# Kernel optimization log

Measured on AMD Instinct MI355X. Metric: run time of the kernel, lower is better.

Reference implementation:

```python
import jax, jax.numpy as jnp
import numpy as np

NUM_CLASSES = 256
EMBED_DIM = 1024
PATCH = 16
LN_EPS = 1e-5


def _sincos_pos_2d(hp, wp, dim):
    # Mirrors SemanticMapTokenizer._build_2d_sincos_pos_embed -> [hp, wp, dim]
    d_h = dim // 2
    d_w = dim - d_h
    d_h_even = (d_h // 2) * 2
    d_w_even = (d_w // 2) * 2

    def one_d(length, d_half):
        pos = jnp.arange(length, dtype=jnp.float32)
        omega = 1.0 / (10000.0 ** (jnp.arange(d_half, dtype=jnp.float32) / d_half))
        out = pos[:, None] * omega[None, :]  # [length, d_half]
        return jnp.concatenate([jnp.sin(out), jnp.cos(out)], axis=1)  # [length, 2*d_half]

    emb_h = one_d(hp, d_h_even // 2)  # [hp, d_h_even]
    emb_w = one_d(wp, d_w_even // 2)  # [wp, d_w_even]
    emb_h = jnp.broadcast_to(emb_h[:, None, :], (hp, wp, d_h_even))
    emb_w = jnp.broadcast_to(emb_w[None, :, :], (hp, wp, d_w_even))
    pos = jnp.concatenate([emb_h, emb_w], axis=-1)
    if pos.shape[-1] < dim:
        pos = jnp.concatenate([pos, jnp.zeros((hp, wp, dim - pos.shape[-1]), jnp.float32)], axis=-1)
    elif pos.shape[-1] > dim:
        pos = pos[:, :, :dim]
    return pos


def setup_inputs() -> dict:
    key = jax.random.key(0)
    k1, k2, k3 = jax.random.split(key, 3)
    semantic_map = jax.random.randint(k1, (2, 1, 512, 512), 0, NUM_CLASSES, dtype=jnp.int32)
    embed_table = jax.random.normal(k2, (NUM_CLASSES, EMBED_DIM), dtype=jnp.float32)
    gamma = jnp.ones((EMBED_DIM,), jnp.float32)
    beta = jnp.zeros((EMBED_DIM,), jnp.float32)
    return {"semantic_map": semantic_map, "embed_table": embed_table, "gamma": gamma, "beta": beta}


def reference(semantic_map, embed_table, gamma, beta):
    b, c, h, w = semantic_map.shape
    p = PATCH
    hp, wp = h // p, w // p
    d = embed_table.shape[1]
    # channel 0, round -> clamp -> int index
    idx = jnp.clip(jnp.round(semantic_map[:, 0].astype(jnp.float32)), 0, NUM_CLASSES - 1).astype(jnp.int32)
    pix = embed_table[idx]  # [B, H, W, D] -- large intermediate (gather)
    # AvgPool2d(kernel=stride=p): mean over non-overlapping p x p patches
    pooled = pix[:, : hp * p, : wp * p, :].reshape(b, hp, p, wp, p, d).mean(axis=(2, 4))  # [B, hp, wp, D]
    pooled = pooled + _sincos_pos_2d(hp, wp, d)[None]
    tokens = pooled.reshape(b, hp * wp, d)
    # LayerNorm over last dim
    mu = tokens.mean(axis=-1, keepdims=True)
    var = jnp.mean(jnp.square(tokens - mu), axis=-1, keepdims=True)
    tokens = (tokens - mu) * jax.lax.rsqrt(var + LN_EPS) * gamma + beta
    return tokens
```

## Files before the change

### kernel.cpp

```cpp
#include <hip/hip_runtime.h>

#define IMG   512
#define NCLS  256
#define DIM   1024
#define HPW   32
#define TPB   8
#define NT2   1024

typedef short bf16x8 __attribute__((ext_vector_type(8)));
typedef float f32x4  __attribute__((ext_vector_type(4)));

__device__ inline ushort bf16rne(float v) {
    unsigned u = __float_as_uint(v);
    return (ushort)((u + 0x7fffu + ((u >> 16) & 1u)) >> 16);
}

__global__ __launch_bounds__(256)
void pack_table(const float* __restrict__ table, ushort* __restrict__ Tt2)
{
    __shared__ ushort tile[16][264];
    const int dtile = blockIdx.x;
    const int d0    = dtile * 16;
    const int t     = threadIdx.x;

    {
        const float* src = table + (size_t)t * DIM + d0;
        #pragma unroll
        for (int q = 0; q < 4; ++q) {
            const float4 v = *reinterpret_cast<const float4*>(src + q * 4);
            tile[q * 4 + 0][t] = bf16rne(v.x);
            tile[q * 4 + 1][t] = bf16rne(v.y);
            tile[q * 4 + 2][t] = bf16rne(v.z);
            tile[q * 4 + 3][t] = bf16rne(v.w);
        }
    }
    __syncthreads();

    const int ks   = t >> 5;
    const int g    = (t >> 3) & 3;
    const int c0   = (t & 7) * 2;
    const int cls0 = ks * 32 + g * 8;
    uint4* dst = reinterpret_cast<uint4*>(Tt2 + (size_t)dtile * 4096 + (size_t)t * 16);
    dst[0] = *reinterpret_cast<const uint4*>(&tile[c0][cls0]);
    dst[1] = *reinterpret_cast<const uint4*>(&tile[c0 + 1][cls0]);
}

__global__ __launch_bounds__(NT2)
void gemm_ln(const int* __restrict__ smap, const ushort* __restrict__ Tt2,
             const float* __restrict__ gamma, const float* __restrict__ beta,
             float* __restrict__ out)
{
    __shared__ unsigned cnt[TPB * NCLS];
    __shared__ ushort   cntb[16][264];
    __shared__ float    red[16][2][4][2];

    const int t    = threadIdx.x;
    const int lane = t & 63;
    const int w    = t >> 6;
    const int c    = lane & 15;
    const int g    = lane >> 4;

    const int tok0 = blockIdx.x * TPB;
    const int b    = tok0 >> 10;
    const int ph   = (tok0 >> 5) & 31;
    const int pw0  = tok0 & 31;

    for (int i = t; i < TPB * NCLS; i += NT2) cnt[i] = 0u;
    for (int i = t; i < 16 * 264; i += NT2) (&cntb[0][0])[i] = 0;
    __syncthreads();

    {
        const int p   = t * 2;
        const int row = p >> 7;
        const int col = p & 127;
        const int2 q = *reinterpret_cast<const int2*>(
            smap + ((size_t)b * IMG + (size_t)(ph * 16 + row)) * IMG + pw0 * 16 + col);
        unsigned* hp = &cnt[(col >> 4) * NCLS];
        atomicAdd(&hp[min(max(q.x, 0), NCLS - 1)], 1u);
        atomicAdd(&hp[min(max(q.y, 0), NCLS - 1)], 1u);
    }
    __syncthreads();

    for (int i = t; i < TPB * NCLS; i += NT2)
        cntb[i >> 8][i & 255] = (ushort)(__float_as_uint((float)cnt[i] * (1.f / 256.f)) >> 16);
    __syncthreads();

    f32x4 acc[4];
    #pragma unroll
    for (int i = 0; i < 4; ++i) acc[i] = (f32x4){0.f, 0.f, 0.f, 0.f};

    const ushort* bt = Tt2 + (size_t)(w * 4) * 4096 + (size_t)lane * 8;
    #pragma unroll 2
    for (int ks = 0; ks < 8; ++ks) {
        const bf16x8 a = *reinterpret_cast<const bf16x8*>(&cntb[c][ks * 32 + g * 8]);
        bf16x8 bfv[4];
        #pragma unroll
        for (int nf = 0; nf < 4; ++nf)
            bfv[nf] = *reinterpret_cast<const bf16x8*>(bt + (size_t)nf * 4096 + ks * 512);
        #pragma unroll
        for (int nf = 0; nf < 4; ++nf)
            acc[nf] = __builtin_amdgcn_mfma_f32_16x16x32_bf16(a, bfv[nf], acc[nf], 0, 0, 0);
    }

    const int quad   = w >> 2;
    const int cosSel = quad & 1;
    float ls[4]  = {0, 0, 0, 0};
    float ls2[4] = {0, 0, 0, 0};

    #pragma unroll
    for (int nf = 0; nf < 4; ++nf) {
        const int dlow = (w & 3) * 64 + nf * 16 + c;
        const float omega = exp2f((float)dlow * (-13.287712379549449f / 256.f));
        if (quad < 2) {
            float sv, cv; __sincosf((float)ph * omega, &sv, &cv);
            const float v = cosSel ? cv : sv;
            #pragma unroll
            for (int i = 0; i < 4; ++i) acc[nf][i] += v;
        } else {
            #pragma unroll
            for (int i = 0; i < 4; ++i) {
                float sv, cv; __sincosf((float)(pw0 + g * 4 + i) * omega, &sv, &cv);
                acc[nf][i] += cosSel ? cv : sv;
            }
        }
        #pragma unroll
        for (int i = 0; i < 4; ++i) { ls[i] += acc[nf][i]; ls2[i] += acc[nf][i] * acc[nf][i]; }
    }

    #pragma unroll
    for (int off = 1; off < 16; off <<= 1) {
        #pragma unroll
        for (int i = 0; i < 4; ++i) {
            ls[i]  += __shfl_xor(ls[i],  off, 64);
            ls2[i] += __shfl_xor(ls2[i], off, 64);
        }
    }
    if (c == 0 && g < 2) {
        #pragma unroll
        for (int i = 0; i < 4; ++i) { red[w][g][i][0] = ls[i]; red[w][g][i][1] = ls2[i]; }
    }
    __syncthreads();

    if (g < 2) {
        float mu[4], rs[4];
        #pragma unroll
        for (int i = 0; i < 4; ++i) {
            float S = 0.f, S2 = 0.f;
            #pragma unroll
            for (int ww = 0; ww < 16; ++ww) { S += red[ww][g][i][0]; S2 += red[ww][g][i][1]; }
            mu[i] = S * (1.f / DIM);
            rs[i] = rsqrtf(S2 * (1.f / DIM) - mu[i] * mu[i] + 1e-5f);
        }
        #pragma unroll
        for (int nf = 0; nf < 4; ++nf) {
            const int d = w * 64 + nf * 16 + c;
            const float gv = gamma[d], bv = beta[d];
            #pragma unroll
            for (int i = 0; i < 4; ++i) {
                const int r = g * 4 + i;
                out[(size_t)(tok0 + r) * DIM + d] = (acc[nf][i] - mu[i]) * rs[i] * gv + bv;
            }
        }
    }
}

extern "C" void kernel_launch(void* const* d_in, const int* in_sizes, int n_in,
                              void* d_out, int out_size, void* d_ws, size_t ws_size,
                              hipStream_t stream) {
    const int*   smap  = (const int*)d_in[0];
    const float* table = (const float*)d_in[1];
    const float* gamma = (const float*)d_in[2];
    const float* beta  = (const float*)d_in[3];
    float*       out   = (float*)d_out;
    ushort*      Tt2   = (ushort*)d_ws;

    const int batches = in_sizes[0] / (IMG * IMG);
    const int tokens  = batches * HPW * HPW;

    pack_table<<<DIM / 16, 256, 0, stream>>>(table, Tt2);
    gemm_ln<<<tokens / TPB, NT2, 0, stream>>>(smap, Tt2, gamma, beta, out);
}
```

Measured before the change: 22.02 us.

## Fuse table packing into GEMM+LN kernel via cooperative grid sync

```diff
diff --git a/kernel.cpp b/kernel.cpp
--- a/kernel.cpp
+++ b/kernel.cpp
@@ -1,11 +1,14 @@
 #include <hip/hip_runtime.h>
+#include <hip/hip_cooperative_groups.h>
+
+namespace cg = cooperative_groups;
 
 #define IMG   512
 #define NCLS  256
 #define DIM   1024
 #define HPW   32
 #define TPB   8
-#define NT2   1024
+#define NT    1024
 
 typedef short bf16x8 __attribute__((ext_vector_type(8)));
 typedef float f32x4  __attribute__((ext_vector_type(4)));
@@ -15,43 +18,14 @@
     return (ushort)((u + 0x7fffu + ((u >> 16) & 1u)) >> 16);
 }
 
-__global__ __launch_bounds__(256)
-void pack_table(const float* __restrict__ table, ushort* __restrict__ Tt2)
-{
-    __shared__ ushort tile[16][264];
-    const int dtile = blockIdx.x;
-    const int d0    = dtile * 16;
-    const int t     = threadIdx.x;
-
-    {
-        const float* src = table + (size_t)t * DIM + d0;
-        #pragma unroll
-        for (int q = 0; q < 4; ++q) {
-            const float4 v = *reinterpret_cast<const float4*>(src + q * 4);
-            tile[q * 4 + 0][t] = bf16rne(v.x);
-            tile[q * 4 + 1][t] = bf16rne(v.y);
-            tile[q * 4 + 2][t] = bf16rne(v.z);
-            tile[q * 4 + 3][t] = bf16rne(v.w);
-        }
-    }
-    __syncthreads();
-
-    const int ks   = t >> 5;
-    const int g    = (t >> 3) & 3;
-    const int c0   = (t & 7) * 2;
-    const int cls0 = ks * 32 + g * 8;
-    uint4* dst = reinterpret_cast<uint4*>(Tt2 + (size_t)dtile * 4096 + (size_t)t * 16);
-    dst[0] = *reinterpret_cast<const uint4*>(&tile[c0][cls0]);
-    dst[1] = *reinterpret_cast<const uint4*>(&tile[c0 + 1][cls0]);
-}
-
-__global__ __launch_bounds__(NT2)
-void gemm_ln(const int* __restrict__ smap, const ushort* __restrict__ Tt2,
-             const float* __restrict__ gamma, const float* __restrict__ beta,
-             float* __restrict__ out)
+__global__ __launch_bounds__(NT)
+void fused_coop(const int* __restrict__ smap, const float* __restrict__ table,
+                const float* __restrict__ gamma, const float* __restrict__ beta,
+                float* __restrict__ out, ushort* __restrict__ Tt2)
 {
     __shared__ unsigned cnt[TPB * NCLS];
     __shared__ ushort   cntb[16][264];
+    __shared__ ushort   tile[16][72];
     __shared__ float    red[16][2][4][2];
 
     const int t    = threadIdx.x;
@@ -60,14 +34,34 @@
     const int c    = lane & 15;
     const int g    = lane >> 4;
 
-    const int tok0 = blockIdx.x * TPB;
+    const int bid  = blockIdx.x;
+    const int tok0 = bid * TPB;
     const int b    = tok0 >> 10;
     const int ph   = (tok0 >> 5) & 31;
     const int pw0  = tok0 & 31;
 
-    for (int i = t; i < TPB * NCLS; i += NT2) cnt[i] = 0u;
-    for (int i = t; i < 16 * 264; i += NT2) (&cntb[0][0])[i] = 0;
+    const int dtile = bid >> 2;
+    const int cq    = bid & 3;
+
+    for (int i = t; i < TPB * NCLS; i += NT) cnt[i] = 0u;
+    for (int i = t; i < 16 * 264; i += NT) (&cntb[0][0])[i] = 0;
+
+    if (t < 256) {
+        const int row = t >> 2, chunk = t & 3;
+        const float4 v = *reinterpret_cast<const float4*>(
+            table + (size_t)(cq * 64 + row) * DIM + dtile * 16 + chunk * 4);
+        tile[chunk * 4 + 0][row] = bf16rne(v.x);
+        tile[chunk * 4 + 1][row] = bf16rne(v.y);
+        tile[chunk * 4 + 2][row] = bf16rne(v.z);
+        tile[chunk * 4 + 3][row] = bf16rne(v.w);
+    }
     __syncthreads();
+
+    {
+        const int cc = (t >> 3) & 15;
+        const int cl = ((t >> 9) << 5) | (((t >> 7) & 3) << 3) | (t & 7);
+        Tt2[(size_t)dtile * 4096 + cq * 1024 + t] = tile[cc][cl];
+    }
 
     {
         const int p   = t * 2;
@@ -81,9 +75,10 @@
     }
     __syncthreads();
 
-    for (int i = t; i < TPB * NCLS; i += NT2)
+    for (int i = t; i < TPB * NCLS; i += NT)
         cntb[i >> 8][i & 255] = (ushort)(__float_as_uint((float)cnt[i] * (1.f / 256.f)) >> 16);
-    __syncthreads();
+
+    cg::this_grid().sync();
 
     f32x4 acc[4];
     #pragma unroll
@@ -176,7 +171,9 @@
 
     const int batches = in_sizes[0] / (IMG * IMG);
     const int tokens  = batches * HPW * HPW;
+    const int nblk    = tokens / TPB;
 
-    pack_table<<<DIM / 16, 256, 0, stream>>>(table, Tt2);
-    gemm_ln<<<tokens / TPB, NT2, 0, stream>>>(smap, Tt2, gamma, beta, out);
+    void* args[] = {(void*)&smap, (void*)&table, (void*)&gamma, (void*)&beta,
+                    (void*)&out, (void*)&Tt2};
+    hipLaunchCooperativeKernel((void*)fused_coop, dim3(nblk), dim3(NT), args, 0, stream);
 }
```

Result: slower. 51.51 us (+134.0%).

## Move histogram building into prep kernel alongside table packing

Applied to the files above, without the earlier changes.

```diff
diff --git a/kernel.cpp b/kernel.cpp
--- a/kernel.cpp
+++ b/kernel.cpp
@@ -16,43 +16,84 @@
 }
 
 __global__ __launch_bounds__(256)
-void pack_table(const float* __restrict__ table, ushort* __restrict__ Tt2)
+void prep(const int* __restrict__ smap, const float* __restrict__ table,
+          ushort* __restrict__ Tt2, ushort* __restrict__ Ab)
 {
-    __shared__ ushort tile[16][264];
-    const int dtile = blockIdx.x;
-    const int d0    = dtile * 16;
-    const int t     = threadIdx.x;
-
-    {
-        const float* src = table + (size_t)t * DIM + d0;
-        #pragma unroll
-        for (int q = 0; q < 4; ++q) {
-            const float4 v = *reinterpret_cast<const float4*>(src + q * 4);
-            tile[q * 4 + 0][t] = bf16rne(v.x);
-            tile[q * 4 + 1][t] = bf16rne(v.y);
-            tile[q * 4 + 2][t] = bf16rne(v.z);
-            tile[q * 4 + 3][t] = bf16rne(v.w);
-        }
-    }
-    __syncthreads();
-
-    const int ks   = t >> 5;
-    const int g    = (t >> 3) & 3;
-    const int c0   = (t & 7) * 2;
-    const int cls0 = ks * 32 + g * 8;
-    uint4* dst = reinterpret_cast<uint4*>(Tt2 + (size_t)dtile * 4096 + (size_t)t * 16);
-    dst[0] = *reinterpret_cast<const uint4*>(&tile[c0][cls0]);
-    dst[1] = *reinterpret_cast<const uint4*>(&tile[c0 + 1][cls0]);
+    __shared__ ushort   tile[16][264];
+    __shared__ unsigned cnt[TPB * NCLS];
+    const int t   = threadIdx.x;
+    const int bid = blockIdx.x;
+
+    if (bid < 64) {
+        const int dtile = bid;
+        const int d0    = dtile * 16;
+        {
+            const float* src = table + (size_t)t * DIM + d0;
+            #pragma unroll
+            for (int q = 0; q < 4; ++q) {
+                const float4 v = *reinterpret_cast<const float4*>(src + q * 4);
+                tile[q * 4 + 0][t] = bf16rne(v.x);
+                tile[q * 4 + 1][t] = bf16rne(v.y);
+                tile[q * 4 + 2][t] = bf16rne(v.z);
+                tile[q * 4 + 3][t] = bf16rne(v.w);
+            }
+        }
+        __syncthreads();
+        const int ks   = t >> 5;
+        const int g    = (t >> 3) & 3;
+        const int c0   = (t & 7) * 2;
+        const int cls0 = ks * 32 + g * 8;
+        uint4* dst = reinterpret_cast<uint4*>(Tt2 + (size_t)dtile * 4096 + (size_t)t * 16);
+        dst[0] = *reinterpret_cast<const uint4*>(&tile[c0][cls0]);
+        dst[1] = *reinterpret_cast<const uint4*>(&tile[c0 + 1][cls0]);
+    } else {
+        const int grp  = bid - 64;
+        const int tok0 = grp * TPB;
+        const int b    = tok0 >> 10;
+        const int ph   = (tok0 >> 5) & 31;
+        const int pw0  = tok0 & 31;
+
+        #pragma unroll
+        for (int i = t; i < TPB * NCLS; i += 256) cnt[i] = 0u;
+        __syncthreads();
+
+        {
+            const int row = t >> 4;
+            const int col = (t & 15) * 8;
+            const int* bp = smap + ((size_t)b * IMG + (size_t)(ph * 16 + row)) * IMG
+                                 + pw0 * 16 + col;
+            const int4 q0 = *reinterpret_cast<const int4*>(bp);
+            const int4 q1 = *reinterpret_cast<const int4*>(bp + 4);
+            unsigned* hp = &cnt[(col >> 4) * NCLS];
+            atomicAdd(&hp[min(max(q0.x, 0), NCLS - 1)], 1u);
+            atomicAdd(&hp[min(max(q0.y, 0), NCLS - 1)], 1u);
+            atomicAdd(&hp[min(max(q0.z, 0), NCLS - 1)], 1u);
+            atomicAdd(&hp[min(max(q0.w, 0), NCLS - 1)], 1u);
+            atomicAdd(&hp[min(max(q1.x, 0), NCLS - 1)], 1u);
+            atomicAdd(&hp[min(max(q1.y, 0), NCLS - 1)], 1u);
+            atomicAdd(&hp[min(max(q1.z, 0), NCLS - 1)], 1u);
+            atomicAdd(&hp[min(max(q1.w, 0), NCLS - 1)], 1u);
+        }
+        __syncthreads();
+
+        ushort* ab = Ab + (size_t)grp * 4096;
+        #pragma unroll
+        for (int i = t; i < 4096; i += 256) {
+            ushort v = 0;
+            if (i < TPB * NCLS)
+                v = (ushort)(__float_as_uint((float)cnt[i] * (1.f / 256.f)) >> 16);
+            ab[i] = v;
+        }
+    }
 }
 
 __global__ __launch_bounds__(NT2)
-void gemm_ln(const int* __restrict__ smap, const ushort* __restrict__ Tt2,
+void gemm_ln(const ushort* __restrict__ Ab, const ushort* __restrict__ Tt2,
              const float* __restrict__ gamma, const float* __restrict__ beta,
              float* __restrict__ out)
 {
-    __shared__ unsigned cnt[TPB * NCLS];
-    __shared__ ushort   cntb[16][264];
-    __shared__ float    red[16][2][4][2];
+    __shared__ ushort cntb[16][264];
+    __shared__ float  red[16][2][4][2];
 
     const int t    = threadIdx.x;
     const int lane = t & 63;
@@ -61,28 +102,14 @@
     const int g    = lane >> 4;
 
     const int tok0 = blockIdx.x * TPB;
-    const int b    = tok0 >> 10;
     const int ph   = (tok0 >> 5) & 31;
     const int pw0  = tok0 & 31;
 
-    for (int i = t; i < TPB * NCLS; i += NT2) cnt[i] = 0u;
-    for (int i = t; i < 16 * 264; i += NT2) (&cntb[0][0])[i] = 0;
-    __syncthreads();
-
     {
-        const int p   = t * 2;
-        const int row = p >> 7;
-        const int col = p & 127;
-        const int2 q = *reinterpret_cast<const int2*>(
-            smap + ((size_t)b * IMG + (size_t)(ph * 16 + row)) * IMG + pw0 * 16 + col);
-        unsigned* hp = &cnt[(col >> 4) * NCLS];
-        atomicAdd(&hp[min(max(q.x, 0), NCLS - 1)], 1u);
-        atomicAdd(&hp[min(max(q.y, 0), NCLS - 1)], 1u);
-    }
-    __syncthreads();
-
-    for (int i = t; i < TPB * NCLS; i += NT2)
-        cntb[i >> 8][i & 255] = (ushort)(__float_as_uint((float)cnt[i] * (1.f / 256.f)) >> 16);
+        const ushort4 v = reinterpret_cast<const ushort4*>(Ab + (size_t)blockIdx.x * 4096)[t];
+        const int idx = t * 4;
+        *reinterpret_cast<ushort4*>(&cntb[idx >> 8][idx & 255]) = v;
+    }
     __syncthreads();
 
     f32x4 acc[4];
@@ -172,11 +199,14 @@
     const float* gamma = (const float*)d_in[2];
     const float* beta  = (const float*)d_in[3];
     float*       out   = (float*)d_out;
-    ushort*      Tt2   = (ushort*)d_ws;
 
     const int batches = in_sizes[0] / (IMG * IMG);
     const int tokens  = batches * HPW * HPW;
-
-    pack_table<<<DIM / 16, 256, 0, stream>>>(table, Tt2);
-    gemm_ln<<<tokens / TPB, NT2, 0, stream>>>(smap, Tt2, gamma, beta, out);
-}
+    const int ngrp    = tokens / TPB;
+
+    ushort* Tt2 = (ushort*)d_ws;
+    ushort* Ab  = Tt2 + (size_t)64 * 4096;
+
+    prep<<<64 + ngrp, 256, 0, stream>>>(smap, table, Tt2, Ab);
+    gemm_ln<<<ngrp, NT2, 0, stream>>>(Ab, Tt2, gamma, beta, out);
+}
```

Measured after the change: 21.87 us. No clear change (-0.7%).
